# Performance work log

Hardware: AMD Instinct MI355X
Metric: run time of the kernel (lower is better)

The kernel has to match this reference:

```python
import jax, jax.numpy as jnp
import numpy as np

B, T, M, D = 4, 512, 16, 128
P, H = 128, 4
E = P // H


def _glorot(k, shape, fan_in, fan_out):
    lim = np.sqrt(6.0 / (fan_in + fan_out)).astype(np.float32)
    return jax.random.uniform(k, shape, jnp.float32, -lim, lim)


def setup_inputs() -> dict:
    key = jax.random.key(0)
    ks = jax.random.split(key, 12)
    inp = jax.random.normal(ks[0], (B, T, M, D), jnp.float32)
    pos = jax.random.normal(ks[1], (B, T, 1, D), jnp.float32)
    # padding mask: valid time steps per batch element (ensures no fully-masked softmax row)
    lengths = jax.random.randint(ks[2], (B,), T // 2, T + 1)
    mask = jnp.broadcast_to(jnp.arange(T)[None, :, None] < lengths[:, None, None], (B, T, M))
    Wq = _glorot(ks[3], (M, P, D), D, P)
    Wk = _glorot(ks[4], (M, P, D), D, P)
    Wv = _glorot(ks[5], (M, P, D), D, P)
    Wq_t = _glorot(ks[6], (M, P, D), D, P)
    Wk_t = _glorot(ks[7], (M, P, D), D, P)
    Bq = jnp.zeros((M, P), jnp.float32)
    Bk = jnp.zeros((M, P), jnp.float32)
    Bv = jnp.zeros((M, P), jnp.float32)
    Bq_t = jnp.zeros((M, P), jnp.float32)
    Bk_t = jnp.zeros((M, P), jnp.float32)
    return {"inp": inp, "pos": pos, "mask": mask,
            "Wq": Wq, "Bq": Bq, "Wk": Wk, "Bk": Bk, "Wv": Wv, "Bv": Bv,
            "Wq_t": Wq_t, "Bq_t": Bq_t, "Wk_t": Wk_t, "Bk_t": Bk_t}


def reference(inp, pos, mask, Wq, Bq, Wk, Bk, Wv, Bv, Wq_t, Bq_t, Wk_t, Bk_t):
    b, t, m, d = inp.shape
    p = Wq.shape[1]
    h, e = H, P // H
    # per-modality projections: (m,p,d) x (b,t,m,d) -> (b,t,m,p)
    q = jnp.einsum('mpd,btmd->btmp', Wq, inp) + Bq
    k = jnp.einsum('mpd,btmd->btmp', Wk, inp) + Bk
    v = jnp.einsum('mpd,btmd->btmp', Wv, inp) + Bv
    pos0 = pos[:, :, 0, :]  # (b,t,d); broadcasts across m
    q_t = jnp.einsum('mpd,btd->btmp', Wq_t, pos0) + Bq_t
    k_t = jnp.einsum('mpd,btd->btmp', Wk_t, pos0) + Bk_t

    def split_heads(x):  # (b,t,m,p) -> (b,m,h,t,e)
        return x.reshape(b, t, m, h, e).transpose(0, 2, 3, 1, 4)

    q, k, v, q_t, k_t = map(split_heads, (q, k, v, q_t, k_t))
    # dual bilinear score: content + positional
    score = (jnp.einsum('bmhte,bmhse->bmhts', q, k)
             + jnp.einsum('bmhte,bmhse->bmhts', q_t, k_t)) / (2.0 * np.sqrt(e).astype(np.float32))
    causal = jnp.tril(jnp.ones((t, t), bool))  # (t,t)
    score = jnp.where(causal, score, -jnp.inf)
    km = mask.transpose(0, 2, 1)[:, :, None, None, :]  # (b,m,1,1,t)
    score = jnp.where(km, score, -jnp.inf)
    w = jax.nn.softmax(score, axis=-1)
    w = jnp.where(km, w, 0.0)
    w = jnp.where(causal, w, 0.0)
    # dropout is identity at inference (drop_rate ignored)
    out = jnp.einsum('bmhts,bmhse->bmhte', w, v)
    return out.transpose(0, 3, 1, 2, 4).reshape(b, t, m, p)
```

## Files before the change

### kernel.cpp

```cpp
#include <hip/hip_runtime.h>

#define Bn 4
#define Tn 512
#define Mn 16
#define Dn 128
#define Pn 128
#define Hn 4
#define SCALE 0.08838834764831845f

#define N4_INP (Bn * Tn * Mn * Dn / 4)
#define N4_POS (Bn * Tn * Dn / 4)
#define N4_W   (Mn * Pn * Dn / 4)
#define WSZ    (Mn * Pn * Dn)
#define CVT_BLOCKS ((N4_INP + N4_POS + 5 * N4_W) / 256)

typedef unsigned short u16;
typedef unsigned int u32;
typedef short s16;
typedef __attribute__((ext_vector_type(8))) s16 bf16x8;
typedef __attribute__((ext_vector_type(4))) float f32x4;

__device__ __forceinline__ u16 f2b(float f) {
  u32 x; __builtin_memcpy(&x, &f, 4);
  x += 0x7fffu + ((x >> 16) & 1u);
  return (u16)(x >> 16);
}
__device__ __forceinline__ u32 pack2(float a, float b) {
  return (u32)f2b(a) | ((u32)f2b(b) << 16);
}
__device__ __forceinline__ bf16x8 ld8(const u16* p) {
  bf16x8 r; __builtin_memcpy(&r, p, 16); return r;
}
__device__ __forceinline__ void st8(u16* p, bf16x8 v) {
  __builtin_memcpy(p, &v, 16);
}
__device__ __forceinline__ f32x4 mfma16(bf16x8 a, bf16x8 b, f32x4 c) {
  return __builtin_amdgcn_mfma_f32_16x16x32_bf16(a, b, c, 0, 0, 0);
}
#define ZERO4 ((f32x4){0.f, 0.f, 0.f, 0.f})

__global__ __launch_bounds__(256) void cvt_kernel(
    const float* __restrict__ inp, const float* __restrict__ pos,
    const float* __restrict__ Wq, const float* __restrict__ Wk,
    const float* __restrict__ Wv, const float* __restrict__ Wqt,
    const float* __restrict__ Wkt,
    const float* __restrict__ Bq, const float* __restrict__ Bk,
    const float* __restrict__ Bv, const float* __restrict__ Bqt,
    const float* __restrict__ Bkt, const void* __restrict__ mask,
    u16* __restrict__ Xbf, u16* __restrict__ Pbf, u16* __restrict__ Wbf,
    float* __restrict__ Bws, int* __restrict__ lens) {
  const int gb = blockIdx.x;
  if (gb < CVT_BLOCKS) {
    const int i = gb * 256 + threadIdx.x;
    const float* src; u16* dst; int off;
    if (i < N4_INP) {
      src = inp; dst = Xbf; off = i;
    } else if (i < N4_INP + N4_POS) {
      src = pos; dst = Pbf; off = i - N4_INP;
    } else {
      const int w = i - (N4_INP + N4_POS);
      const int tsel = w >> 16;
      off = w & 65535;
      dst = Wbf + tsel * WSZ;
      src = (tsel == 0) ? Wq : (tsel == 1) ? Wk : (tsel == 2) ? Wv
          : (tsel == 3) ? Wqt : Wkt;
    }
    const float4 v = ((const float4*)src)[off];
    ushort4 o;
    o.x = f2b(v.x); o.y = f2b(v.y); o.z = f2b(v.z); o.w = f2b(v.w);
    ((ushort4*)dst)[off] = o;
  } else if (gb == CVT_BLOCKS) {
    for (int i = threadIdx.x; i < 5 * Mn * Pn; i += 256) {
      const int arr = i >> 11, idx = i & 2047;
      const float* src = (arr == 0) ? Bq : (arr == 1) ? Bk : (arr == 2) ? Bv
                       : (arr == 3) ? Bqt : Bkt;
      Bws[i] = src[idx];
    }
  } else {
    const int b = threadIdx.x >> 6, lane = threadIdx.x & 63;
    const u32 w0 = ((const u32*)mask)[0];
    const int mode = (w0 == 1u) ? 0 : (w0 == 0x3F800000u) ? 1
                   : (w0 == 0x3F803F80u) ? 2 : 3;
    int c = 0;
    for (int t = lane; t < Tn; t += 64) {
      const size_t idx = ((size_t)b * Tn + t) * Mn;
      int nz;
      if (mode == 0)      nz = (((const int*)mask)[idx] != 0);
      else if (mode == 1) nz = (((const u32*)mask)[idx] != 0u);
      else if (mode == 2) nz = (((const u16*)mask)[idx] != 0);
      else                nz = (((const unsigned char*)mask)[idx] != 0);
      c += nz;
    }
    for (int o = 32; o; o >>= 1) c += __shfl_xor(c, o);
    if (lane == 0) lens[b] = c;
  }
}

__global__ __launch_bounds__(256, 2) void proj_mfma(
    const u16* __restrict__ Xbf, const u16* __restrict__ Pbf,
    const u16* __restrict__ Wbf, const float* __restrict__ Bws,
    u16* __restrict__ Qa, u16* __restrict__ Ka, u16* __restrict__ Qb,
    u16* __restrict__ Kb, u16* __restrict__ Vt) {
  __shared__ __align__(16) u16 slab_all[4][4][32][40];

  const int tid = threadIdx.x;
  const int wv = tid >> 6, lane = tid & 63;
  const int quad = lane >> 4, l16 = lane & 15;
  const int wu = blockIdx.x * 4 + wv;

  const int tsel = wu % 5;
  const int rest = wu / 5;
  const int m = rest & (Mn - 1);
  const int rg = rest >> 4;
  const int bt0 = rg * 32;
  const int tl = bt0 & (Tn - 1);
  const int b = bt0 >> 9;
  const int bmh0 = (b * Mn + m) * Hn;
  u16 (*slab)[32][40] = slab_all[wv];

  const u16* W = Wbf + tsel * WSZ + m * Pn * Dn;
  const float* bias = Bws + tsel * 2048 + m * Pn;
  const int usepos = (tsel >= 3);

  f32x4 acc[2][8];
#pragma unroll
  for (int tt = 0; tt < 2; ++tt)
#pragma unroll
    for (int n = 0; n < 8; ++n) acc[tt][n] = ZERO4;

#pragma unroll
  for (int kc = 0; kc < 4; ++kc) {
    const int ko = kc * 32 + quad * 8;
    bf16x8 x0, x1;
    if (usepos) {
      x0 = ld8(Pbf + (size_t)(bt0 + l16) * Dn + ko);
      x1 = ld8(Pbf + (size_t)(bt0 + 16 + l16) * Dn + ko);
    } else {
      x0 = ld8(Xbf + ((size_t)(bt0 + l16) * Mn + m) * Dn + ko);
      x1 = ld8(Xbf + ((size_t)(bt0 + 16 + l16) * Mn + m) * Dn + ko);
    }
#pragma unroll
    for (int n = 0; n < 8; ++n) {
      const bf16x8 w = ld8(W + (size_t)(n * 16 + l16) * Dn + ko);
      acc[0][n] = mfma16(x0, w, acc[0][n]);
      acc[1][n] = mfma16(x1, w, acc[1][n]);
    }
  }

  if (tsel == 2) {
#pragma unroll
    for (int n = 0; n < 8; ++n) {
      const int np = n >> 1;
      const int e_loc = (n & 1) * 16 + l16;
      const float bv = bias[n * 16 + l16];
#pragma unroll
      for (int tt = 0; tt < 2; ++tt) {
        const int t_loc = tt * 16 + quad * 4;
        uint2 d;
        d.x = pack2(acc[tt][n][0] + bv, acc[tt][n][1] + bv);
        d.y = pack2(acc[tt][n][2] + bv, acc[tt][n][3] + bv);
        *(uint2*)&slab[np][e_loc][t_loc] = d;
      }
    }
#pragma unroll
    for (int np = 0; np < 4; ++np)
#pragma unroll
      for (int i = 0; i < 2; ++i) {
        const int c = i * 64 + lane;
        const int e_loc = c >> 2, sub = c & 3;
        const bf16x8 v = ld8(&slab[np][e_loc][sub * 8]);
        st8(Vt + ((size_t)(bmh0 + np) * 32 + e_loc) * Tn + tl + sub * 8, v);
      }
  } else {
    u16* dst = (tsel == 0) ? Qa : (tsel == 1) ? Ka : (tsel == 3) ? Qb : Kb;
    const float sc = (tsel == 0 || tsel == 3) ? SCALE : 1.f;
#pragma unroll
    for (int n = 0; n < 8; ++n) {
      const int np = n >> 1;
      const int e = (n & 1) * 16 + l16;
      const float bv = bias[n * 16 + l16];
#pragma unroll
      for (int tt = 0; tt < 2; ++tt)
#pragma unroll
        for (int reg = 0; reg < 4; ++reg) {
          const int t_loc = tt * 16 + quad * 4 + reg;
          slab[np][t_loc][e] = f2b((acc[tt][n][reg] + bv) * sc);
        }
    }
#pragma unroll
    for (int np = 0; np < 4; ++np)
#pragma unroll
      for (int i = 0; i < 2; ++i) {
        const int c = i * 64 + lane;
        const int t_loc = c >> 2, sub = c & 3;
        const bf16x8 v = ld8(&slab[np][t_loc][sub * 8]);
        st8(dst + ((size_t)(bmh0 + np) * Tn + tl + t_loc) * 32 + sub * 8, v);
      }
  }
}

__global__ __launch_bounds__(256, 4) void attn_flash(
    const u16* __restrict__ Qa, const u16* __restrict__ Ka,
    const u16* __restrict__ Qb, const u16* __restrict__ Kb,
    const u16* __restrict__ Vt, const int* __restrict__ lens,
    float* __restrict__ out) {
  __shared__ __align__(16) u16 Ps[4 * 32 * 72];

  const int tid = threadIdx.x;
  const int wv = tid >> 6, lane = tid & 63;
  const int quad = lane >> 4, l16 = lane & 15;

  const int wu = blockIdx.x * 4 + wv;
  const int qt = wu & 15;
  const int bmh = wu >> 4;
  const int b = bmh >> 6;
  const int len = lens[b];
  const int q0 = qt * 32;

  const size_t rowbase = (size_t)bmh * Tn;
  const size_t vbase = (size_t)bmh * 32 * Tn;
  u16* myPs = &Ps[wv * 32 * 72];

  bf16x8 qf[2][2];
#pragma unroll
  for (int qs = 0; qs < 2; ++qs) {
    const size_t r = (rowbase + q0 + qs * 16 + l16) * 32 + quad * 8;
    qf[qs][0] = ld8(Qa + r);
    qf[qs][1] = ld8(Qb + r);
  }

  f32x4 O[2][2];
#pragma unroll
  for (int qs = 0; qs < 2; ++qs)
#pragma unroll
    for (int es = 0; es < 2; ++es) O[qs][es] = ZERO4;
  float mrow[2] = {-1e30f, -1e30f}, lsum[2] = {0.f, 0.f};

  const int s_hi = min(q0 + 32, len);
  for (int s0 = 0; s0 < s_hi; s0 += 64) {
    f32x4 S[2][4];
#pragma unroll
    for (int st = 0; st < 4; ++st) {
      const size_t kr = (rowbase + s0 + st * 16 + l16) * 32 + quad * 8;
      const bf16x8 k0 = ld8(Ka + kr);
      const bf16x8 k1 = ld8(Kb + kr);
#pragma unroll
      for (int qs = 0; qs < 2; ++qs)
        S[qs][st] = mfma16(k1, qf[qs][1], mfma16(k0, qf[qs][0], ZERO4));
    }

#pragma unroll
    for (int qs = 0; qs < 2; ++qs) {
      const int q = q0 + qs * 16 + l16;
      const int qcap = min(q, len - 1);
      const int sb = s0 + quad * 4;
      float cmax = -1e30f;
#pragma unroll
      for (int st = 0; st < 4; ++st)
#pragma unroll
        for (int reg = 0; reg < 4; ++reg) {
          const int s = sb + st * 16 + reg;
          const float v = (s <= qcap) ? S[qs][st][reg] : -1e30f;
          S[qs][st][reg] = v;
          cmax = fmaxf(cmax, v);
        }
      cmax = fmaxf(cmax, __shfl_xor(cmax, 16));
      cmax = fmaxf(cmax, __shfl_xor(cmax, 32));
      const float mnew = fmaxf(mrow[qs], cmax);
      const float alpha = __expf(mrow[qs] - mnew);
      mrow[qs] = mnew;
      float rsum = 0.f;
      u32 pk[4][2];
#pragma unroll
      for (int st = 0; st < 4; ++st) {
        const float p0 = __expf(S[qs][st][0] - mnew);
        const float p1 = __expf(S[qs][st][1] - mnew);
        const float p2 = __expf(S[qs][st][2] - mnew);
        const float p3 = __expf(S[qs][st][3] - mnew);
        rsum += (p0 + p1) + (p2 + p3);
        pk[st][0] = pack2(p0, p1);
        pk[st][1] = pack2(p2, p3);
      }
      rsum += __shfl_xor(rsum, 16);
      rsum += __shfl_xor(rsum, 32);
      lsum[qs] = lsum[qs] * alpha + rsum;
#pragma unroll
      for (int es = 0; es < 2; ++es)
#pragma unroll
        for (int reg = 0; reg < 4; ++reg) O[qs][es][reg] *= alpha;
#pragma unroll
      for (int st = 0; st < 4; ++st) {
        uint2 d; d.x = pk[st][0]; d.y = pk[st][1];
        *(uint2*)&myPs[(qs * 16 + l16) * 72 + st * 16 + quad * 4] = d;
      }
    }

#pragma unroll
    for (int kc = 0; kc < 2; ++kc) {
      const int ko = kc * 32 + quad * 8;
      const bf16x8 pf0 = ld8(&myPs[l16 * 72 + ko]);
      const bf16x8 pf1 = ld8(&myPs[(16 + l16) * 72 + ko]);
      const bf16x8 vf0 = ld8(Vt + vbase + (size_t)l16 * Tn + s0 + ko);
      const bf16x8 vf1 = ld8(Vt + vbase + (size_t)(16 + l16) * Tn + s0 + ko);
      O[0][0] = mfma16(vf0, pf0, O[0][0]);
      O[0][1] = mfma16(vf1, pf0, O[0][1]);
      O[1][0] = mfma16(vf0, pf1, O[1][0]);
      O[1][1] = mfma16(vf1, pf1, O[1][1]);
    }
  }

  const int mm = (bmh >> 2) & (Mn - 1);
  const int h = bmh & (Hn - 1);
#pragma unroll
  for (int qs = 0; qs < 2; ++qs) {
    const float linv = 1.0f / lsum[qs];
    const int t = q0 + qs * 16 + l16;
    const size_t ob = (((size_t)b * Tn + t) * Mn + mm) * Pn + h * 32 + quad * 4;
#pragma unroll
    for (int es = 0; es < 2; ++es) {
      float4 o;
      o.x = O[qs][es][0] * linv; o.y = O[qs][es][1] * linv;
      o.z = O[qs][es][2] * linv; o.w = O[qs][es][3] * linv;
      *(float4*)&out[ob + es * 16] = o;
    }
  }
}

extern "C" void kernel_launch(void* const* d_in, const int* in_sizes, int n_in,
                              void* d_out, int out_size, void* d_ws, size_t ws_size,
                              hipStream_t stream) {
  const float* inp = (const float*)d_in[0];
  const float* pos = (const float*)d_in[1];
  const void* mask = d_in[2];
  const float* Wq  = (const float*)d_in[3];
  const float* Bq  = (const float*)d_in[4];
  const float* Wk  = (const float*)d_in[5];
  const float* Bk  = (const float*)d_in[6];
  const float* Wv  = (const float*)d_in[7];
  const float* Bv  = (const float*)d_in[8];
  const float* Wqt = (const float*)d_in[9];
  const float* Bqt = (const float*)d_in[10];
  const float* Wkt = (const float*)d_in[11];
  const float* Bkt = (const float*)d_in[12];
  float* out = (float*)d_out;

  const size_t nA = (size_t)Bn * Mn * Hn * Tn * 32;
  u16* Qa = (u16*)d_ws;
  u16* Ka = Qa + nA;
  u16* Qb = Ka + nA;
  u16* Kb = Qb + nA;
  u16* Vt = Kb + nA;
  u16* Xbf = Vt + nA;
  u16* Pbf = Xbf + (size_t)Bn * Tn * Mn * Dn;
  u16* Wbf = Pbf + (size_t)Bn * Tn * Dn;
  float* Bws = (float*)(Wbf + 5 * (size_t)WSZ);
  int* lens = (int*)(Bws + 5 * 2048);

  cvt_kernel<<<CVT_BLOCKS + 2, 256, 0, stream>>>(
      inp, pos, Wq, Wk, Wv, Wqt, Wkt, Bq, Bk, Bv, Bqt, Bkt, mask,
      Xbf, Pbf, Wbf, Bws, lens);
  proj_mfma<<<5120 / 4, 256, 0, stream>>>(Xbf, Pbf, Wbf, Bws, Qa, Ka, Qb, Kb, Vt);
  attn_flash<<<Bn * Mn * Hn * (Tn / 32) / 4, 256, 0, stream>>>(
      Qa, Ka, Qb, Kb, Vt, lens, out);
}
```

Measured before the change: 163.8 us.

## Fuse fp32-to-bf16 conversion into projection kernel and skip masking on full tiles

Removes the separate conversion kernel. The projection kernel now reads fp32 inputs and weights directly and converts them to bf16 in registers, and the mask-length computation moves into an extra block of the same launch. This drops one launch and a full write and re-read of the bf16 copies of the input and weights, but each wave now reads twice the bytes and weights are converted repeatedly across waves. In attention, causal and padding masking is skipped for 64-wide key tiles that lie entirely below the diagonal and inside the valid length, which saves compares and selects in the inner loop.

```diff
diff --git a/kernel.cpp b/kernel.cpp
--- a/kernel.cpp
+++ b/kernel.cpp
@@ -8,12 +8,6 @@
 #define Hn 4
 #define SCALE 0.08838834764831845f
 
-#define N4_INP (Bn * Tn * Mn * Dn / 4)
-#define N4_POS (Bn * Tn * Dn / 4)
-#define N4_W   (Mn * Pn * Dn / 4)
-#define WSZ    (Mn * Pn * Dn)
-#define CVT_BLOCKS ((N4_INP + N4_POS + 5 * N4_W) / 256)
-
 typedef unsigned short u16;
 typedef unsigned int u32;
 typedef short s16;
@@ -34,12 +28,20 @@
 __device__ __forceinline__ void st8(u16* p, bf16x8 v) {
   __builtin_memcpy(p, &v, 16);
 }
+__device__ __forceinline__ bf16x8 ldcvt8(const float* p) {
+  const float4 a = *(const float4*)p;
+  const float4 b = *(const float4*)(p + 4);
+  bf16x8 r; u32* r32 = (u32*)&r;
+  r32[0] = pack2(a.x, a.y); r32[1] = pack2(a.z, a.w);
+  r32[2] = pack2(b.x, b.y); r32[3] = pack2(b.z, b.w);
+  return r;
+}
 __device__ __forceinline__ f32x4 mfma16(bf16x8 a, bf16x8 b, f32x4 c) {
   return __builtin_amdgcn_mfma_f32_16x16x32_bf16(a, b, c, 0, 0, 0);
 }
 #define ZERO4 ((f32x4){0.f, 0.f, 0.f, 0.f})
 
-__global__ __launch_bounds__(256) void cvt_kernel(
+__global__ __launch_bounds__(256, 2) void proj_fused(
     const float* __restrict__ inp, const float* __restrict__ pos,
     const float* __restrict__ Wq, const float* __restrict__ Wk,
     const float* __restrict__ Wv, const float* __restrict__ Wqt,
@@ -47,43 +49,18 @@
     const float* __restrict__ Bq, const float* __restrict__ Bk,
     const float* __restrict__ Bv, const float* __restrict__ Bqt,
     const float* __restrict__ Bkt, const void* __restrict__ mask,
-    u16* __restrict__ Xbf, u16* __restrict__ Pbf, u16* __restrict__ Wbf,
-    float* __restrict__ Bws, int* __restrict__ lens) {
-  const int gb = blockIdx.x;
-  if (gb < CVT_BLOCKS) {
-    const int i = gb * 256 + threadIdx.x;
-    const float* src; u16* dst; int off;
-    if (i < N4_INP) {
-      src = inp; dst = Xbf; off = i;
-    } else if (i < N4_INP + N4_POS) {
-      src = pos; dst = Pbf; off = i - N4_INP;
-    } else {
-      const int w = i - (N4_INP + N4_POS);
-      const int tsel = w >> 16;
-      off = w & 65535;
-      dst = Wbf + tsel * WSZ;
-      src = (tsel == 0) ? Wq : (tsel == 1) ? Wk : (tsel == 2) ? Wv
-          : (tsel == 3) ? Wqt : Wkt;
-    }
-    const float4 v = ((const float4*)src)[off];
-    ushort4 o;
-    o.x = f2b(v.x); o.y = f2b(v.y); o.z = f2b(v.z); o.w = f2b(v.w);
-    ((ushort4*)dst)[off] = o;
-  } else if (gb == CVT_BLOCKS) {
-    for (int i = threadIdx.x; i < 5 * Mn * Pn; i += 256) {
-      const int arr = i >> 11, idx = i & 2047;
-      const float* src = (arr == 0) ? Bq : (arr == 1) ? Bk : (arr == 2) ? Bv
-                       : (arr == 3) ? Bqt : Bkt;
-      Bws[i] = src[idx];
-    }
-  } else {
-    const int b = threadIdx.x >> 6, lane = threadIdx.x & 63;
+    u16* __restrict__ Qa, u16* __restrict__ Ka, u16* __restrict__ Qb,
+    u16* __restrict__ Kb, u16* __restrict__ Vt, int* __restrict__ lens) {
+  const int tid = threadIdx.x;
+  const int wv = tid >> 6, lane = tid & 63;
+
+  if (blockIdx.x == 1280) {
     const u32 w0 = ((const u32*)mask)[0];
     const int mode = (w0 == 1u) ? 0 : (w0 == 0x3F800000u) ? 1
                    : (w0 == 0x3F803F80u) ? 2 : 3;
     int c = 0;
     for (int t = lane; t < Tn; t += 64) {
-      const size_t idx = ((size_t)b * Tn + t) * Mn;
+      const size_t idx = ((size_t)wv * Tn + t) * Mn;
       int nz;
       if (mode == 0)      nz = (((const int*)mask)[idx] != 0);
       else if (mode == 1) nz = (((const u32*)mask)[idx] != 0u);
@@ -92,22 +69,14 @@
       c += nz;
     }
     for (int o = 32; o; o >>= 1) c += __shfl_xor(c, o);
-    if (lane == 0) lens[b] = c;
-  }
-}
-
-__global__ __launch_bounds__(256, 2) void proj_mfma(
-    const u16* __restrict__ Xbf, const u16* __restrict__ Pbf,
-    const u16* __restrict__ Wbf, const float* __restrict__ Bws,
-    u16* __restrict__ Qa, u16* __restrict__ Ka, u16* __restrict__ Qb,
-    u16* __restrict__ Kb, u16* __restrict__ Vt) {
+    if (lane == 0) lens[wv] = c;
+    return;
+  }
+
   __shared__ __align__(16) u16 slab_all[4][4][32][40];
 
-  const int tid = threadIdx.x;
-  const int wv = tid >> 6, lane = tid & 63;
   const int quad = lane >> 4, l16 = lane & 15;
   const int wu = blockIdx.x * 4 + wv;
-
   const int tsel = wu % 5;
   const int rest = wu / 5;
   const int m = rest & (Mn - 1);
@@ -118,8 +87,12 @@
   const int bmh0 = (b * Mn + m) * Hn;
   u16 (*slab)[32][40] = slab_all[wv];
 
-  const u16* W = Wbf + tsel * WSZ + m * Pn * Dn;
-  const float* bias = Bws + tsel * 2048 + m * Pn;
+  const float* W = (tsel == 0) ? Wq : (tsel == 1) ? Wk : (tsel == 2) ? Wv
+                 : (tsel == 3) ? Wqt : Wkt;
+  const float* Bb = (tsel == 0) ? Bq : (tsel == 1) ? Bk : (tsel == 2) ? Bv
+                  : (tsel == 3) ? Bqt : Bkt;
+  W += (size_t)m * Pn * Dn;
+  const float* bias = Bb + m * Pn;
   const int usepos = (tsel >= 3);
 
   f32x4 acc[2][8];
@@ -133,15 +106,15 @@
     const int ko = kc * 32 + quad * 8;
     bf16x8 x0, x1;
     if (usepos) {
-      x0 = ld8(Pbf + (size_t)(bt0 + l16) * Dn + ko);
-      x1 = ld8(Pbf + (size_t)(bt0 + 16 + l16) * Dn + ko);
+      x0 = ldcvt8(pos + (size_t)(bt0 + l16) * Dn + ko);
+      x1 = ldcvt8(pos + (size_t)(bt0 + 16 + l16) * Dn + ko);
     } else {
-      x0 = ld8(Xbf + ((size_t)(bt0 + l16) * Mn + m) * Dn + ko);
-      x1 = ld8(Xbf + ((size_t)(bt0 + 16 + l16) * Mn + m) * Dn + ko);
+      x0 = ldcvt8(inp + ((size_t)(bt0 + l16) * Mn + m) * Dn + ko);
+      x1 = ldcvt8(inp + ((size_t)(bt0 + 16 + l16) * Mn + m) * Dn + ko);
     }
 #pragma unroll
     for (int n = 0; n < 8; ++n) {
-      const bf16x8 w = ld8(W + (size_t)(n * 16 + l16) * Dn + ko);
+      const bf16x8 w = ldcvt8(W + (size_t)(n * 16 + l16) * Dn + ko);
       acc[0][n] = mfma16(x0, w, acc[0][n]);
       acc[1][n] = mfma16(x1, w, acc[1][n]);
     }
@@ -249,21 +222,27 @@
         S[qs][st] = mfma16(k1, qf[qs][1], mfma16(k0, qf[qs][0], ZERO4));
     }
 
+    const bool full = (s0 + 63 <= q0) && (s0 + 63 < len);
+
 #pragma unroll
     for (int qs = 0; qs < 2; ++qs) {
-      const int q = q0 + qs * 16 + l16;
-      const int qcap = min(q, len - 1);
-      const int sb = s0 + quad * 4;
+      if (!full) {
+        const int q = q0 + qs * 16 + l16;
+        const int qcap = min(q, len - 1);
+        const int sb = s0 + quad * 4;
+#pragma unroll
+        for (int st = 0; st < 4; ++st)
+#pragma unroll
+          for (int reg = 0; reg < 4; ++reg) {
+            const int s = sb + st * 16 + reg;
+            S[qs][st][reg] = (s <= qcap) ? S[qs][st][reg] : -1e30f;
+          }
+      }
       float cmax = -1e30f;
 #pragma unroll
       for (int st = 0; st < 4; ++st)
 #pragma unroll
-        for (int reg = 0; reg < 4; ++reg) {
-          const int s = sb + st * 16 + reg;
-          const float v = (s <= qcap) ? S[qs][st][reg] : -1e30f;
-          S[qs][st][reg] = v;
-          cmax = fmaxf(cmax, v);
-        }
+        for (int reg = 0; reg < 4; ++reg) cmax = fmaxf(cmax, S[qs][st][reg]);
       cmax = fmaxf(cmax, __shfl_xor(cmax, 16));
       cmax = fmaxf(cmax, __shfl_xor(cmax, 32));
       const float mnew = fmaxf(mrow[qs], cmax);
@@ -350,16 +329,11 @@
   u16* Qb = Ka + nA;
   u16* Kb = Qb + nA;
   u16* Vt = Kb + nA;
-  u16* Xbf = Vt + nA;
-  u16* Pbf = Xbf + (size_t)Bn * Tn * Mn * Dn;
-  u16* Wbf = Pbf + (size_t)Bn * Tn * Dn;
-  float* Bws = (float*)(Wbf + 5 * (size_t)WSZ);
-  int* lens = (int*)(Bws + 5 * 2048);
-
-  cvt_kernel<<<CVT_BLOCKS + 2, 256, 0, stream>>>(
+  int* lens = (int*)(Vt + nA);
+
+  proj_fused<<<1281, 256, 0, stream>>>(
       inp, pos, Wq, Wk, Wv, Wqt, Wkt, Bq, Bk, Bv, Bqt, Bkt, mask,
-      Xbf, Pbf, Wbf, Bws, lens);
-  proj_mfma<<<5120 / 4, 256, 0, stream>>>(Xbf, Pbf, Wbf, Bws, Qa, Ka, Qb, Kb, Vt);
+      Qa, Ka, Qb, Kb, Vt, lens);
   attn_flash<<<Bn * Mn * Hn * (Tn / 32) / 4, 256, 0, stream>>>(
       Qa, Ka, Qb, Kb, Vt, lens, out);
 }
```

After: 176.2 us. +7.6%, slower.
